# Optimization experiments

Measured on AMD Instinct MI355X. Metric: run time of the kernel, lower is better.

Reference implementation:

```python
import jax, jax.numpy as jnp
import numpy as np
import math

B, S, DIM = 2, 2048, 2048
H, KV, HD = 16, 1, 128  # query heads, kv heads, head dim


def setup_inputs() -> dict:
    key = jax.random.key(0)
    ks = jax.random.split(key, 6)
    std = 0.02
    return {
        "hidden_states": jax.random.normal(ks[0], (B, S, DIM), jnp.float32),
        "attention_mask": jnp.zeros((B, 1, S, S), jnp.float32),
        "wq": jax.random.normal(ks[1], (DIM, H * HD), jnp.float32) * std,
        "bq": jnp.zeros((H * HD,), jnp.float32),
        "wk": jax.random.normal(ks[2], (DIM, KV * HD), jnp.float32) * std,
        "bk": jnp.zeros((KV * HD,), jnp.float32),
        "wv": jax.random.normal(ks[3], (DIM, KV * HD), jnp.float32) * std,
        "bv": jnp.zeros((KV * HD,), jnp.float32),
        "wo": jax.random.normal(ks[4], (H * HD, DIM), jnp.float32) * std,
        "bo": jnp.zeros((DIM,), jnp.float32),
    }


def reference(hidden_states, attention_mask, wq, bq, wk, bk, wv, bv, wo, bo):
    b, s, _ = hidden_states.shape
    q = (hidden_states @ wq + bq).reshape(b, s, H, HD)
    k = (hidden_states @ wk + bk).reshape(b, s, KV, HD)
    v = (hidden_states @ wv + bv).reshape(b, s, KV, HD)
    # [b, h, s, d]
    q = jnp.transpose(q, (0, 2, 1, 3))
    k = jnp.transpose(k, (0, 2, 1, 3))
    v = jnp.transpose(v, (0, 2, 1, 3))
    # broadcast shared KV heads to all query heads (num_kv_heads < num_query_heads)
    repeats = H // KV
    k = jnp.repeat(k, repeats, axis=1)
    v = jnp.repeat(v, repeats, axis=1)
    scores = jnp.einsum('bhqd,bhkd->bhqk', q, k) / math.sqrt(HD)
    scores = scores + attention_mask
    weights = jax.nn.softmax(scores, axis=-1)
    attn = jnp.einsum('bhqk,bhkd->bhqd', weights, v)
    attn = jnp.transpose(attn, (0, 2, 1, 3)).reshape(b, s, H * HD)
    return attn @ wo + bo
```

## Files before the change

kernel.cpp:

```cpp
#include <hip/hip_runtime.h>
#include <hip/hip_bf16.h>
#include <stdint.h>

#define S_LEN 2048
#define DIMSZ 2048
#define NH    16
#define HD    128
#define NQK   2176
#define NQKV  2304

typedef short  bf16x8  __attribute__((ext_vector_type(8)));
typedef float  floatx4 __attribute__((ext_vector_type(4)));
typedef float  floatx16 __attribute__((ext_vector_type(16)));
typedef int    intx4   __attribute__((ext_vector_type(4)));
typedef unsigned short u16;

#define mfma32 __builtin_amdgcn_mfma_f32_32x32x16_bf16
#define LOG2E 1.4426950408889634f

__device__ __forceinline__ u16 f2bf(float x) {
  unsigned int u = __builtin_bit_cast(unsigned int, x);
  u = (u + 0x7FFFu + ((u >> 16) & 1u)) >> 16;
  return (u16)u;
}

__device__ __forceinline__ int cvtpk(float lo, float hi) {
  int r;
  asm("v_cvt_pk_bf16_f32 %0, %1, %2" : "=v"(r) : "v"(lo), "v"(hi));
  return r;
}

#if __has_builtin(__builtin_amdgcn_exp2f)
__device__ __forceinline__ float fexp2(float x) { return __builtin_amdgcn_exp2f(x); }
#else
__device__ __forceinline__ float fexp2(float x) { return exp2f(x); }
#endif

#if __has_builtin(__builtin_amdgcn_permlane32_swap)
__device__ __forceinline__ void half_swap(int& a, int& b) {
  auto r = __builtin_amdgcn_permlane32_swap(a, b, false, false);
  a = (int)r[0]; b = (int)r[1];
}
__device__ __forceinline__ float red_max32(float x) {
  int xi = __builtin_bit_cast(int, x);
  auto r = __builtin_amdgcn_permlane32_swap(xi, xi, false, false);
  return fmaxf(__builtin_bit_cast(float, (int)r[0]), __builtin_bit_cast(float, (int)r[1]));
}
__device__ __forceinline__ float red_add32(float x) {
  int xi = __builtin_bit_cast(int, x);
  auto r = __builtin_amdgcn_permlane32_swap(xi, xi, false, false);
  return __builtin_bit_cast(float, (int)r[0]) + __builtin_bit_cast(float, (int)r[1]);
}
#else
__device__ __forceinline__ void half_swap(int& a, int& b) {
  int as = __shfl_xor(a, 32);
  int bs = __shfl_xor(b, 32);
  int lane = threadIdx.x & 63;
  int na = (lane < 32) ? a : bs;
  int nb = (lane < 32) ? as : b;
  a = na; b = nb;
}
__device__ __forceinline__ float red_max32(float x) { return fmaxf(x, __shfl_xor(x, 32)); }
__device__ __forceinline__ float red_add32(float x) { return x + __shfl_xor(x, 32); }
#endif

__device__ __forceinline__ void gload16(const void* g, void* l) {
  __builtin_amdgcn_global_load_lds(
      reinterpret_cast<const __attribute__((address_space(1))) void*>(reinterpret_cast<uintptr_t>(g)),
      reinterpret_cast<__attribute__((address_space(3))) void*>(reinterpret_cast<uintptr_t>(l)),
      16, 0, 0);
}

__global__ void k_cvt_bf16(const float* __restrict__ in, u16* __restrict__ out, int n4) {
  int i = blockIdx.x * blockDim.x + threadIdx.x;
  if (i < n4) {
    float4 v = ((const float4*)in)[i];
    ushort4 o;
    o.x = f2bf(v.x); o.y = f2bf(v.y); o.z = f2bf(v.z); o.w = f2bf(v.w);
    ((ushort4*)out)[i] = o;
  }
}

__global__ void k_transpose_bf16(const float* __restrict__ in, u16* __restrict__ out,
                                 int K, int N, int rowOff) {
  __shared__ float t[64][65];
  int c0 = blockIdx.x * 64;
  int r0 = blockIdx.y * 64;
  int tid = threadIdx.x;
  int lr = tid >> 6;
  int lc = tid & 63;
#pragma unroll
  for (int i = 0; i < 16; ++i) {
    int r = lr + i * 4;
    t[r][lc] = in[(size_t)(r0 + r) * N + c0 + lc];
  }
  __syncthreads();
#pragma unroll
  for (int i = 0; i < 16; ++i) {
    int r = lr + i * 4;
    out[(size_t)(rowOff + c0 + r) * K + r0 + lc] = f2bf(t[lc][r]);
  }
}

__global__ void k_bias_concat(const float* __restrict__ bq, const float* __restrict__ bk,
                              const float* __restrict__ bv, float* __restrict__ out) {
  int i = blockIdx.x * 256 + threadIdx.x;
  if (i < NQKV) out[i] = (i < 2048) ? bq[i] : (i < NQK ? bk[i - 2048] : bv[i - NQK]);
}

__device__ __forceinline__ void stage_tile(const u16* __restrict__ G, int ldg, int row0, int kt,
                                           u16* lbase, int wid, int lane) {
#pragma unroll
  for (int i = 0; i < 4; ++i) {
    int c   = (wid * 4 + i) * 64 + lane;
    int row = c >> 3, cin = c & 7;
    int cs  = cin ^ (row & 7);
    const u16* g = G + (size_t)(row0 + row) * ldg + kt * 64 + cs * 8;
    gload16(g, (char*)lbase + (wid * 4 + i) * 1024);
  }
}

template <int OMODE>
__global__ __launch_bounds__(256)
void k_gemm(const u16* __restrict__ A, const u16* __restrict__ Bt,
            const float* __restrict__ bias, void* __restrict__ Cout,
            u16* __restrict__ vt, int M, int N, int K) {
  __shared__ u16 lA[2][128 * 64];
  __shared__ u16 lB[2][128 * 64];
  const int tid = threadIdx.x, lane = tid & 63, wid = tid >> 6;
  const int wm = wid >> 1, wn = wid & 1;
  const int tm = blockIdx.x, tn = blockIdx.y;
  const int nk = K >> 6;

  stage_tile(A, K, tm * 128, 0, lA[0], wid, lane);
  stage_tile(Bt, K, tn * 128, 0, lB[0], wid, lane);
  __syncthreads();

  floatx4 acc[4][4] = {};
  int buf = 0;
  for (int kt = 0; kt < nk; ++kt) {
    if (kt + 1 < nk) {
      stage_tile(A, K, tm * 128, kt + 1, lA[buf ^ 1], wid, lane);
      stage_tile(Bt, K, tn * 128, kt + 1, lB[buf ^ 1], wid, lane);
    }
    const char* pa = (const char*)&lA[buf][0];
    const char* pb = (const char*)&lB[buf][0];
#pragma unroll
    for (int kk = 0; kk < 2; ++kk) {
      bf16x8 af[4], bfr[4];
      int gch = kk * 4 + (lane >> 4);
#pragma unroll
      for (int f = 0; f < 4; ++f) {
        int ra = wm * 64 + f * 16 + (lane & 15);
        af[f]  = *(const bf16x8*)(pa + ra * 128 + ((gch ^ (ra & 7)) << 4));
        int rb = wn * 64 + f * 16 + (lane & 15);
        bfr[f] = *(const bf16x8*)(pb + rb * 128 + ((gch ^ (rb & 7)) << 4));
      }
      __builtin_amdgcn_s_setprio(1);
#pragma unroll
      for (int fm = 0; fm < 4; ++fm)
#pragma unroll
        for (int fn = 0; fn < 4; ++fn)
          acc[fm][fn] = __builtin_amdgcn_mfma_f32_16x16x32_bf16(af[fm], bfr[fn], acc[fm][fn], 0, 0, 0);
      __builtin_amdgcn_s_setprio(0);
    }
    __syncthreads();
    buf ^= 1;
  }

#pragma unroll
  for (int fm = 0; fm < 4; ++fm)
#pragma unroll
    for (int fn = 0; fn < 4; ++fn)
#pragma unroll
      for (int r = 0; r < 4; ++r) {
        int rowg = tm * 128 + wm * 64 + fm * 16 + (lane >> 4) * 4 + r;
        int colg = tn * 128 + wn * 64 + fn * 16 + (lane & 15);
        float v = acc[fm][fn][r] + bias[colg];
        if constexpr (OMODE == 1) {
          ((float*)Cout)[(size_t)rowg * N + colg] = v;
        } else {
          if (colg < NQK) {
            ((u16*)Cout)[(size_t)rowg * N + colg] = f2bf(v);
          } else {
            int d = colg - NQK;
            int bg = rowg >> 11, s = rowg & 2047;
            vt[((size_t)bg * HD + d) * S_LEN + s] = f2bf(v);
          }
        }
      }
}

__device__ __forceinline__ void stage_kv(const u16* __restrict__ qkv, const u16* __restrict__ vt,
                                         int b, int kt, u16* lK, u16* lV, int wid, int lane) {
#pragma unroll
  for (int i = 0; i < 2; ++i) {
    int seg = wid * 2 + i;
    {
      int r = seg * 4 + (lane >> 4), cin = lane & 15;
      const u16* g = qkv + (size_t)(b * S_LEN + kt * 64 + r) * NQKV + 2048 + ((cin ^ (r & 7)) * 8);
      gload16(g, (char*)lK + seg * 1024);
    }
    {
      int r = seg * 8 + (lane >> 3), cin = lane & 7;
      const u16* g = vt + ((size_t)b * HD + r) * S_LEN + kt * 64 + ((cin ^ (r & 7)) * 8);
      gload16(g, (char*)lV + seg * 1024);
    }
  }
}

__global__ __launch_bounds__(512)
void k_attn(const u16* __restrict__ qkv, const u16* __restrict__ vt,
            const float* __restrict__ mask, u16* __restrict__ attn) {
  __shared__ __align__(16) u16   lK[2][64 * 128];
  __shared__ __align__(16) u16   lV[2][128 * 64];
  __shared__ __align__(16) float lM[2][32 * 64];
  const int tid = threadIdx.x, lane = tid & 63, wid = tid >> 6;
  const int qt = blockIdx.x, hg = blockIdx.y, b = blockIdx.z;
  const int h = hg * 8 + wid;
  const int q = lane & 31, h5 = lane >> 5;
  const float c_sl2 = 0.08838834764831845f * LOG2E;

  bf16x8 qf[8];
  const size_t qrow = (size_t)(b * S_LEN + qt * 32 + q);
#pragma unroll
  for (int cs = 0; cs < 8; ++cs)
    qf[cs] = *(const bf16x8*)(qkv + qrow * NQKV + h * HD + cs * 16 + h5 * 8);

  float m_ = -1e30f, l_ = 0.f;
  floatx16 acco[4] = {};

  const int mq = tid >> 4, mc = tid & 15;
  const float* mrow = mask + (size_t)b * S_LEN * S_LEN + (size_t)(qt * 32 + mq) * S_LEN + mc * 4;

  stage_kv(qkv, vt, b, 0, lK[0], lV[0], wid, lane);
  floatx4 mreg = *(const floatx4*)(mrow);
  *(floatx4*)((char*)&lM[0][0] + mq * 256 + ((mc ^ (mq & 7)) << 4)) = mreg * LOG2E;
  __syncthreads();

  int buf = 0;
  for (int kt = 0; kt < S_LEN / 64; ++kt) {
    if (kt + 1 < S_LEN / 64) {
      stage_kv(qkv, vt, b, kt + 1, lK[buf ^ 1], lV[buf ^ 1], wid, lane);
      mreg = *(const floatx4*)(mrow + (size_t)(kt + 1) * 64);
    }

    floatx16 accs0 = {}, accs1 = {};
    const char* pK = (const char*)&lK[buf][0];
    __builtin_amdgcn_s_setprio(1);
#pragma unroll
    for (int cs = 0; cs < 8; ++cs) {
      int c = cs * 2 + h5;
      bf16x8 kf0 = *(const bf16x8*)(pK + q * 256 + ((c ^ (q & 7)) << 4));
      bf16x8 kf1 = *(const bf16x8*)(pK + (32 + q) * 256 + ((c ^ (q & 7)) << 4));
      accs0 = mfma32(kf0, qf[cs], accs0, 0, 0, 0);
      accs1 = mfma32(kf1, qf[cs], accs1, 0, 0, 0);
    }
    __builtin_amdgcn_s_setprio(0);

    float pr[32];
    float rowm = -1e30f;
    const char* pM = (const char*)&lM[buf][0];
#pragma unroll
    for (int kb = 0; kb < 2; ++kb)
#pragma unroll
      for (int rg = 0; rg < 4; ++rg) {
        int c = kb * 8 + rg * 2 + h5;
        floatx4 m4 = *(const floatx4*)(pM + q * 256 + ((c ^ (q & 7)) << 4));
#pragma unroll
        for (int t = 0; t < 4; ++t) {
          float sv = (kb ? accs1[rg * 4 + t] : accs0[rg * 4 + t]) * c_sl2 + m4[t];
          pr[kb * 16 + rg * 4 + t] = sv;
          rowm = fmaxf(rowm, sv);
        }
      }
    rowm = red_max32(rowm);
    if (__any(rowm > m_ + 11.5415603f)) {
      float mn = fmaxf(m_, rowm);
      float al = fexp2(m_ - mn);
      m_ = mn;
      l_ *= al;
#pragma unroll
      for (int dt = 0; dt < 4; ++dt) acco[dt] *= al;
    }
    float sum = 0.f;
#pragma unroll
    for (int j = 0; j < 32; ++j) {
      float e = fexp2(pr[j] - m_);
      pr[j] = e;
      sum += e;
    }
    l_ += red_add32(sum);

    bf16x8 pf[4];
#pragma unroll
    for (int kb = 0; kb < 2; ++kb)
#pragma unroll
      for (int s = 0; s < 2; ++s) {
        int base = kb * 16 + s * 8;
        int A0 = cvtpk(pr[base + 0], pr[base + 1]);
        int A1 = cvtpk(pr[base + 2], pr[base + 3]);
        int B0 = cvtpk(pr[base + 4], pr[base + 5]);
        int B1 = cvtpk(pr[base + 6], pr[base + 7]);
        half_swap(A0, B0);
        half_swap(A1, B1);
        intx4 w;
        w[0] = A0; w[1] = A1; w[2] = B0; w[3] = B1;
        pf[kb * 2 + s] = __builtin_bit_cast(bf16x8, w);
      }

    const char* pV = (const char*)&lV[buf][0];
    __builtin_amdgcn_s_setprio(1);
#pragma unroll
    for (int dt = 0; dt < 4; ++dt) {
      int rd = dt * 32 + q;
#pragma unroll
      for (int ks = 0; ks < 4; ++ks) {
        int c = ks * 2 + h5;
        bf16x8 vf = *(const bf16x8*)(pV + rd * 128 + ((c ^ (q & 7)) << 4));
        acco[dt] = mfma32(vf, pf[ks], acco[dt], 0, 0, 0);
      }
    }
    __builtin_amdgcn_s_setprio(0);

    if (kt + 1 < S_LEN / 64)
      *(floatx4*)((char*)&lM[buf ^ 1][0] + mq * 256 + ((mc ^ (mq & 7)) << 4)) = mreg * LOG2E;
    __syncthreads();
    buf ^= 1;
  }

  float inv = 1.0f / l_;
  u16* obase = attn + qrow * DIMSZ + h * HD;
#pragma unroll
  for (int dt = 0; dt < 4; ++dt)
#pragma unroll
    for (int rg = 0; rg < 4; ++rg) {
      int d0 = dt * 32 + rg * 8 + h5 * 4;
      ushort4 st;
      st.x = f2bf(acco[dt][rg * 4 + 0] * inv);
      st.y = f2bf(acco[dt][rg * 4 + 1] * inv);
      st.z = f2bf(acco[dt][rg * 4 + 2] * inv);
      st.w = f2bf(acco[dt][rg * 4 + 3] * inv);
      *(ushort4*)(obase + d0) = st;
    }
}

extern "C" void kernel_launch(void* const* d_in, const int* in_sizes, int n_in,
                              void* d_out, int out_size, void* d_ws, size_t ws_size,
                              hipStream_t stream) {
  const float* hidden = (const float*)d_in[0];
  const float* mask   = (const float*)d_in[1];
  const float* wq = (const float*)d_in[2];
  const float* bq = (const float*)d_in[3];
  const float* wk = (const float*)d_in[4];
  const float* bk = (const float*)d_in[5];
  const float* wv = (const float*)d_in[6];
  const float* bv = (const float*)d_in[7];
  const float* wo = (const float*)d_in[8];
  const float* bo = (const float*)d_in[9];
  float* out = (float*)d_out;

  char* ws = (char*)d_ws;
  u16*   hb    = (u16*)(ws);
  u16*   wqkvT = (u16*)(ws + 16777216);
  u16*   woT   = (u16*)(ws + 26214400);
  float* bqkv  = (float*)(ws + 34603008);
  u16*   qkv   = (u16*)(ws + 34612224);
  u16*   vt    = (u16*)(ws + 53486592);
  u16*   attn  = (u16*)(ws + 54535168);

  k_cvt_bf16<<<dim3(8192), dim3(256), 0, stream>>>(hidden, hb, 4096 * 2048 / 4);
  k_transpose_bf16<<<dim3(32, 32), dim3(256), 0, stream>>>(wq, wqkvT, 2048, 2048, 0);
  k_transpose_bf16<<<dim3(2, 32),  dim3(256), 0, stream>>>(wk, wqkvT, 2048, 128, 2048);
  k_transpose_bf16<<<dim3(2, 32),  dim3(256), 0, stream>>>(wv, wqkvT, 2048, 128, NQK);
  k_transpose_bf16<<<dim3(32, 32), dim3(256), 0, stream>>>(wo, woT, 2048, 2048, 0);
  k_bias_concat<<<dim3(9), dim3(256), 0, stream>>>(bq, bk, bv, bqkv);

  k_gemm<0><<<dim3(32, 18), dim3(256), 0, stream>>>(hb, wqkvT, bqkv, (void*)qkv, vt, 4096, NQKV, 2048);
  k_attn<<<dim3(64, 2, 2), dim3(512), 0, stream>>>(qkv, vt, mask, attn);
  k_gemm<1><<<dim3(32, 16), dim3(256), 0, stream>>>(attn, woT, bo, (void*)out, (u16*)nullptr, 4096, 2048, 2048);
}
```

Measured before the change: 204.7 us.

## Enlarge GEMM tiles to 256x128, shrink attention blocks, read mask directly into registers

```diff
diff --git a/kernel.cpp b/kernel.cpp
--- a/kernel.cpp
+++ b/kernel.cpp
@@ -108,40 +108,41 @@
   if (i < NQKV) out[i] = (i < 2048) ? bq[i] : (i < NQK ? bk[i - 2048] : bv[i - NQK]);
 }
 
+template <int NSEG>
 __device__ __forceinline__ void stage_tile(const u16* __restrict__ G, int ldg, int row0, int kt,
                                            u16* lbase, int wid, int lane) {
 #pragma unroll
-  for (int i = 0; i < 4; ++i) {
-    int c   = (wid * 4 + i) * 64 + lane;
+  for (int i = 0; i < NSEG; ++i) {
+    int c   = (wid * NSEG + i) * 64 + lane;
     int row = c >> 3, cin = c & 7;
     int cs  = cin ^ (row & 7);
     const u16* g = G + (size_t)(row0 + row) * ldg + kt * 64 + cs * 8;
-    gload16(g, (char*)lbase + (wid * 4 + i) * 1024);
+    gload16(g, (char*)lbase + (wid * NSEG + i) * 1024);
   }
 }
 
 template <int OMODE>
-__global__ __launch_bounds__(256)
+__global__ __launch_bounds__(512)
 void k_gemm(const u16* __restrict__ A, const u16* __restrict__ Bt,
             const float* __restrict__ bias, void* __restrict__ Cout,
             u16* __restrict__ vt, int M, int N, int K) {
-  __shared__ u16 lA[2][128 * 64];
+  __shared__ u16 lA[2][256 * 64];
   __shared__ u16 lB[2][128 * 64];
   const int tid = threadIdx.x, lane = tid & 63, wid = tid >> 6;
   const int wm = wid >> 1, wn = wid & 1;
   const int tm = blockIdx.x, tn = blockIdx.y;
   const int nk = K >> 6;
 
-  stage_tile(A, K, tm * 128, 0, lA[0], wid, lane);
-  stage_tile(Bt, K, tn * 128, 0, lB[0], wid, lane);
+  stage_tile<4>(A, K, tm * 256, 0, lA[0], wid, lane);
+  stage_tile<2>(Bt, K, tn * 128, 0, lB[0], wid, lane);
   __syncthreads();
 
   floatx4 acc[4][4] = {};
   int buf = 0;
   for (int kt = 0; kt < nk; ++kt) {
     if (kt + 1 < nk) {
-      stage_tile(A, K, tm * 128, kt + 1, lA[buf ^ 1], wid, lane);
-      stage_tile(Bt, K, tn * 128, kt + 1, lB[buf ^ 1], wid, lane);
+      stage_tile<4>(A, K, tm * 256, kt + 1, lA[buf ^ 1], wid, lane);
+      stage_tile<2>(Bt, K, tn * 128, kt + 1, lB[buf ^ 1], wid, lane);
     }
     const char* pa = (const char*)&lA[buf][0];
     const char* pb = (const char*)&lB[buf][0];
@@ -174,7 +175,7 @@
     for (int fn = 0; fn < 4; ++fn)
 #pragma unroll
       for (int r = 0; r < 4; ++r) {
-        int rowg = tm * 128 + wm * 64 + fm * 16 + (lane >> 4) * 4 + r;
+        int rowg = tm * 256 + wm * 64 + fm * 16 + (lane >> 4) * 4 + r;
         int colg = tn * 128 + wn * 64 + fn * 16 + (lane & 15);
         float v = acc[fm][fn][r] + bias[colg];
         if constexpr (OMODE == 1) {
@@ -194,8 +195,8 @@
 __device__ __forceinline__ void stage_kv(const u16* __restrict__ qkv, const u16* __restrict__ vt,
                                          int b, int kt, u16* lK, u16* lV, int wid, int lane) {
 #pragma unroll
-  for (int i = 0; i < 2; ++i) {
-    int seg = wid * 2 + i;
+  for (int i = 0; i < 4; ++i) {
+    int seg = wid * 4 + i;
     {
       int r = seg * 4 + (lane >> 4), cin = lane & 15;
       const u16* g = qkv + (size_t)(b * S_LEN + kt * 64 + r) * NQKV + 2048 + ((cin ^ (r & 7)) * 8);
@@ -209,17 +210,16 @@
   }
 }
 
-__global__ __launch_bounds__(512)
+__global__ __launch_bounds__(256)
 void k_attn(const u16* __restrict__ qkv, const u16* __restrict__ vt,
             const float* __restrict__ mask, u16* __restrict__ attn) {
-  __shared__ __align__(16) u16   lK[2][64 * 128];
-  __shared__ __align__(16) u16   lV[2][128 * 64];
-  __shared__ __align__(16) float lM[2][32 * 64];
+  __shared__ __align__(16) u16 lK[2][64 * 128];
+  __shared__ __align__(16) u16 lV[2][128 * 64];
   const int tid = threadIdx.x, lane = tid & 63, wid = tid >> 6;
   const int qt = blockIdx.x, hg = blockIdx.y, b = blockIdx.z;
-  const int h = hg * 8 + wid;
+  const int h = hg * 4 + wid;
   const int q = lane & 31, h5 = lane >> 5;
-  const float c_sl2 = 0.08838834764831845f * LOG2E;
+  const float scale = 0.08838834764831845f;
 
   bf16x8 qf[8];
   const size_t qrow = (size_t)(b * S_LEN + qt * 32 + q);
@@ -227,23 +227,25 @@
   for (int cs = 0; cs < 8; ++cs)
     qf[cs] = *(const bf16x8*)(qkv + qrow * NQKV + h * HD + cs * 16 + h5 * 8);
 
+  const float* mptr = mask + ((size_t)b * S_LEN + qt * 32 + q) * S_LEN + h5 * 4;
+
   float m_ = -1e30f, l_ = 0.f;
   floatx16 acco[4] = {};
 
-  const int mq = tid >> 4, mc = tid & 15;
-  const float* mrow = mask + (size_t)b * S_LEN * S_LEN + (size_t)(qt * 32 + mq) * S_LEN + mc * 4;
-
   stage_kv(qkv, vt, b, 0, lK[0], lV[0], wid, lane);
-  floatx4 mreg = *(const floatx4*)(mrow);
-  *(floatx4*)((char*)&lM[0][0] + mq * 256 + ((mc ^ (mq & 7)) << 4)) = mreg * LOG2E;
   __syncthreads();
 
   int buf = 0;
   for (int kt = 0; kt < S_LEN / 64; ++kt) {
-    if (kt + 1 < S_LEN / 64) {
+    if (kt + 1 < S_LEN / 64)
       stage_kv(qkv, vt, b, kt + 1, lK[buf ^ 1], lV[buf ^ 1], wid, lane);
-      mreg = *(const floatx4*)(mrow + (size_t)(kt + 1) * 64);
-    }
+
+    floatx4 mk[8];
+#pragma unroll
+    for (int kb = 0; kb < 2; ++kb)
+#pragma unroll
+      for (int rg = 0; rg < 4; ++rg)
+        mk[kb * 4 + rg] = *(const floatx4*)(mptr + kt * 64 + kb * 32 + rg * 8);
 
     floatx16 accs0 = {}, accs1 = {};
     const char* pK = (const char*)&lK[buf][0];
@@ -260,33 +262,32 @@
 
     float pr[32];
     float rowm = -1e30f;
-    const char* pM = (const char*)&lM[buf][0];
 #pragma unroll
     for (int kb = 0; kb < 2; ++kb)
 #pragma unroll
       for (int rg = 0; rg < 4; ++rg) {
-        int c = kb * 8 + rg * 2 + h5;
-        floatx4 m4 = *(const floatx4*)(pM + q * 256 + ((c ^ (q & 7)) << 4));
+        floatx4 m4 = mk[kb * 4 + rg];
 #pragma unroll
         for (int t = 0; t < 4; ++t) {
-          float sv = (kb ? accs1[rg * 4 + t] : accs0[rg * 4 + t]) * c_sl2 + m4[t];
+          float sv = (kb ? accs1[rg * 4 + t] : accs0[rg * 4 + t]) * scale + m4[t];
           pr[kb * 16 + rg * 4 + t] = sv;
           rowm = fmaxf(rowm, sv);
         }
       }
     rowm = red_max32(rowm);
-    if (__any(rowm > m_ + 11.5415603f)) {
+    if (__any(rowm > m_ + 8.0f)) {
       float mn = fmaxf(m_, rowm);
-      float al = fexp2(m_ - mn);
+      float al = fexp2((m_ - mn) * LOG2E);
       m_ = mn;
       l_ *= al;
 #pragma unroll
       for (int dt = 0; dt < 4; ++dt) acco[dt] *= al;
     }
+    float nml2 = -m_ * LOG2E;
     float sum = 0.f;
 #pragma unroll
     for (int j = 0; j < 32; ++j) {
-      float e = fexp2(pr[j] - m_);
+      float e = fexp2(pr[j] * LOG2E + nml2);
       pr[j] = e;
       sum += e;
     }
@@ -323,8 +324,6 @@
     }
     __builtin_amdgcn_s_setprio(0);
 
-    if (kt + 1 < S_LEN / 64)
-      *(floatx4*)((char*)&lM[buf ^ 1][0] + mq * 256 + ((mc ^ (mq & 7)) << 4)) = mreg * LOG2E;
     __syncthreads();
     buf ^= 1;
   }
@@ -376,7 +375,7 @@
   k_transpose_bf16<<<dim3(32, 32), dim3(256), 0, stream>>>(wo, woT, 2048, 2048, 0);
   k_bias_concat<<<dim3(9), dim3(256), 0, stream>>>(bq, bk, bv, bqkv);
 
-  k_gemm<0><<<dim3(32, 18), dim3(256), 0, stream>>>(hb, wqkvT, bqkv, (void*)qkv, vt, 4096, NQKV, 2048);
-  k_attn<<<dim3(64, 2, 2), dim3(512), 0, stream>>>(qkv, vt, mask, attn);
-  k_gemm<1><<<dim3(32, 16), dim3(256), 0, stream>>>(attn, woT, bo, (void*)out, (u16*)nullptr, 4096, 2048, 2048);
-}
+  k_gemm<0><<<dim3(16, 18), dim3(512), 0, stream>>>(hb, wqkvT, bqkv, (void*)qkv, vt, 4096, NQKV, 2048);
+  k_attn<<<dim3(64, 4, 2), dim3(256), 0, stream>>>(qkv, vt, mask, attn);
+  k_gemm<1><<<dim3(16, 16), dim3(512), 0, stream>>>(attn, woT, bo, (void*)out, (u16*)nullptr, 4096, 2048, 2048);
+}
```

Measured after the change: 303.8 us. 1.48x slower.
